# Optimization experiments

Hardware: AMD Instinct MI355X
Metric: run time of the kernel (lower is better)

Reference implementation:

```python
import jax, jax.numpy as jnp
import numpy as np

D = 64
NU = 30000
NI = 20000
LU = 50  # mailbox length at user nodes (item_max_length)
LI = 50  # mailbox length at item nodes (user_max_length)


def setup_inputs() -> dict:
    key = jax.random.key(0)
    ks = jax.random.split(key, 14)
    s = 0.05
    return {
        "user_feat": jax.random.normal(ks[0], (NU, D), jnp.float32),
        "item_feat": jax.random.normal(ks[1], (NI, D), jnp.float32),
        "W_u": jax.random.normal(ks[2], (D, D), jnp.float32) * s,
        "W_i": jax.random.normal(ks[3], (D, D), jnp.float32) * s,
        "Wg_u": jax.random.normal(ks[4], (2 * D, D), jnp.float32) * s,
        "Wg_i": jax.random.normal(ks[5], (2 * D, D), jnp.float32) * s,
        "i_te": jax.random.normal(ks[6], (LI, D), jnp.float32) * s,
        "i_te_k": jax.random.normal(ks[7], (LI, D), jnp.float32) * s,
        "u_te": jax.random.normal(ks[8], (LU, D), jnp.float32) * s,
        "u_te_k": jax.random.normal(ks[9], (LU, D), jnp.float32) * s,
        "item_nbr": jax.random.randint(ks[10], (NI, LI), 0, NU, jnp.int32),
        "item_time": jax.random.randint(ks[11], (NI, LI), 0, 1000000, jnp.int32),
        "user_nbr": jax.random.randint(ks[12], (NU, LU), 0, NI, jnp.int32),
        "user_time": jax.random.randint(ks[13], (NU, LU), 0, 1000000, jnp.int32),
    }


def _orgat_att(src_mb, dst_h, time, te, te_k):
    """One DGSR reduce: long-term time-encoded attention + short-term last-attention.
    src_mb: [N, L, d] gathered source features; dst_h: [N, d]; time: [N, L] int.
    Returns concat([h_long, h_short]) @ Wg applied by caller.
    """
    L = time.shape[1]
    d = src_mb.shape[-1]
    scale = jnp.sqrt(jnp.asarray(d, src_mb.dtype))
    # rank of each edge's time within the neighborhood; re_order: 0 = most recent
    rank = jnp.argsort(jnp.argsort(time, axis=1), axis=1)
    re_o = L - rank - 1                                       # [N, L]
    e = jnp.sum((te[re_o] + src_mb) * dst_h[:, None, :], axis=2) / scale
    alpha = jax.nn.softmax(e, axis=1)                         # [N, L]
    h_long = jnp.sum(alpha[..., None] * (src_mb + te_k[re_o]), axis=1)
    # short-term: attention keyed on the most-recent neighbor
    last = jnp.argmax(time, axis=1)
    last_em = jnp.take_along_axis(src_mb, last[:, None, None], axis=1)  # [N,1,d]
    e1 = jnp.sum(last_em * src_mb, axis=2) / scale
    a1 = jax.nn.softmax(e1, axis=1)
    h_short = jnp.sum(a1[..., None] * src_mb, axis=1)
    return jnp.concatenate([h_long, h_short], axis=-1)        # [N, 2d]


def reference(user_feat, item_feat, W_u, W_i, Wg_u, Wg_i, i_te, i_te_k,
              u_te, u_te_k, item_nbr, item_time, user_nbr, user_time):
    uh = user_feat @ W_u   # user_weight (feat_drop=0)
    ih = item_feat @ W_i   # item_weight
    # 'by' edges: users -> items (item reduce uses user mailboxes + i_time_encoding)
    u_mb = uh[item_nbr]                                        # [NI, LI, d]
    item_new = _orgat_att(u_mb, ih, item_time, i_te, i_te_k) @ Wg_i
    # 'pby' edges: items -> users (user reduce uses item mailboxes + u_time_encoding)
    i_mb = ih[user_nbr]                                        # [NU, LU, d]
    user_new = _orgat_att(i_mb, uh, user_time, u_te, u_te_k) @ Wg_u
    # residual update functions
    user_out = jax.nn.elu(user_new + user_feat)
    item_out = jax.nn.elu(item_new + item_feat)
    return user_out, item_out
```

## Files before the change

### kernel.cpp

```cpp
#include <hip/hip_runtime.h>
#include <stdint.h>

#define D   64
#define L   50
#define NUM_U 30000
#define NUM_I 20000
#define MROWS 50
#define PW3 (MROWS * 32 + 96 + 192)
#define GEMM_BLKS 782


typedef __attribute__((ext_vector_type(8))) short short8x;
typedef __attribute__((ext_vector_type(4))) float f32x4;

__device__ __forceinline__ float lof(unsigned int u) {
    union { unsigned int i; float f; } v; v.i = u << 16; return v.f;
}
__device__ __forceinline__ float hif(unsigned int u) {
    union { unsigned int i; float f; } v; v.i = u & 0xffff0000u; return v.f;
}
__device__ __forceinline__ unsigned int f2bfbits(float f) {
    union { float f; unsigned int i; } v; v.f = f;
    return (v.i + 0x7fffu + ((v.i >> 16) & 1u)) >> 16;
}
__device__ __forceinline__ unsigned int packbf(float a, float b) {
    return f2bfbits(a) | (f2bfbits(b) << 16);
}
__device__ __forceinline__ float rl(float v, int l) {
    return __int_as_float(__builtin_amdgcn_readlane(__float_as_int(v), l));
}
__device__ __forceinline__ int rli(int v, int l) {
    return __builtin_amdgcn_readlane(v, l);
}
__device__ __forceinline__ void gload_lds16(const void* g, void* l) {
    __builtin_amdgcn_global_load_lds(
        (const __attribute__((address_space(1))) unsigned int*)g,
        (__attribute__((address_space(3))) unsigned int*)l, 16, 0, 0);
}

__global__ __launch_bounds__(256) void prep(
    const float* __restrict__ user_feat, const float* __restrict__ item_feat,
    const float* __restrict__ W_u, const float* __restrict__ W_i,
    const float* __restrict__ Wg_i, const float* __restrict__ Wg_u,
    const float* __restrict__ te_i, const float* __restrict__ te_u,
    const float* __restrict__ tk_i, const float* __restrict__ tk_u,
    unsigned int* __restrict__ H,
    unsigned short* __restrict__ WgPi, unsigned short* __restrict__ WgPu,
    unsigned short* __restrict__ tePi, unsigned short* __restrict__ tePu,
    unsigned short* __restrict__ tkPi, unsigned short* __restrict__ tkPu)
{
    const int tid = threadIdx.x;
    if (blockIdx.x < GEMM_BLKS) {
        const int lane = tid & 63, wid = tid >> 6;
        const int tile = blockIdx.x * 4 + wid;
        if (tile >= 3125) return;
        const int r0 = tile * 16;
        const float* src; const float* W;
        if (r0 < NUM_U) { src = user_feat + (size_t)r0 * D;            W = W_u; }
        else            { src = item_feat + (size_t)(r0 - NUM_U) * D;  W = W_i; }
        const int q4 = lane >> 4, c16 = lane & 15;

        short8x bf[2];
#pragma unroll
        for (int kt = 0; kt < 2; kt++) {
            const float* fp = src + c16 * D + kt * 32 + q4 * 8;
            float4 x = *(const float4*)fp;
            float4 y = *(const float4*)(fp + 4);
            union { short8x v; unsigned int u[4]; } t2;
            t2.u[0] = packbf(x.x, x.y); t2.u[1] = packbf(x.z, x.w);
            t2.u[2] = packbf(y.x, y.y); t2.u[3] = packbf(y.z, y.w);
            bf[kt] = t2.v;
        }
        f32x4 zero4 = {0.f, 0.f, 0.f, 0.f};
        f32x4 acc[4];
#pragma unroll
        for (int mt = 0; mt < 4; mt++) acc[mt] = zero4;
#pragma unroll
        for (int kt = 0; kt < 2; kt++) {
#pragma unroll
            for (int mt = 0; mt < 4; mt++) {
                union { short8x v; unsigned short u[8]; } a;
#pragma unroll
                for (int j = 0; j < 8; j++)
                    a.u[j] = (unsigned short)f2bfbits(
                        W[(kt * 32 + q4 * 8 + j) * D + c16 + 16 * mt]);
                acc[mt] = __builtin_amdgcn_mfma_f32_16x16x32_bf16(a.v, bf[kt], acc[mt], 0, 0, 0);
            }
        }
        unsigned int* Hrow = H + (size_t)(r0 + c16) * 32;
#pragma unroll
        for (int mt = 0; mt < 4; mt++) {
            uint2 pk;
            pk.x = packbf(acc[mt][0], acc[mt][1]);
            pk.y = packbf(acc[mt][2], acc[mt][3]);
            *(uint2*)(Hrow + 8 * mt + 2 * q4) = pk;
        }
    } else {
        int gid = (blockIdx.x - GEMM_BLKS) * 256 + tid;
        for (int idx = gid; idx < 8192; idx += 4096) {
            int n = idx >> 7, k = idx & 127;
            WgPi[idx] = (unsigned short)f2bfbits(Wg_i[k * 64 + n]);
            WgPu[idx] = (unsigned short)f2bfbits(Wg_u[k * 64 + n]);
        }
        {
            int idx = gid;
            int r = idx >> 6, k = idx & 63;
            tePi[idx] = (r < L) ? (unsigned short)f2bfbits(te_i[r * 64 + k]) : 0;
            tePu[idx] = (r < L) ? (unsigned short)f2bfbits(te_u[r * 64 + k]) : 0;
            int d = idx >> 6, rr = idx & 63;
            tkPi[idx] = (rr < L) ? (unsigned short)f2bfbits(tk_i[rr * 64 + d]) : 0;
            tkPu[idx] = (rr < L) ? (unsigned short)f2bfbits(tk_u[rr * 64 + d]) : 0;
        }
    }
}

__global__ __launch_bounds__(256, 5) void attn_fused(
    const unsigned int* __restrict__ H,
    const float* __restrict__ user_feat, const float* __restrict__ item_feat,
    const unsigned short* __restrict__ WgPi, const unsigned short* __restrict__ WgPu,
    const unsigned short* __restrict__ tePi, const unsigned short* __restrict__ tePu,
    const unsigned short* __restrict__ tkPi, const unsigned short* __restrict__ tkPu,
    const int* __restrict__ item_nbr, const int* __restrict__ item_time,
    const int* __restrict__ user_nbr, const int* __restrict__ user_time,
    float* __restrict__ out)
{
    __shared__ unsigned int lds[4 * PW3];

    const int tid = threadIdx.x, lane = tid & 63, wid = tid >> 6;
    const bool iside = blockIdx.x < (NUM_I / 4);
    const int bb = iside ? blockIdx.x : blockIdx.x - NUM_I / 4;
    const int n = bb * 4 + wid;
    const int src_base = iside ? 0 : NUM_U;
    const int dst_base = iside ? NUM_U : 0;
    const float* dst_feat = iside ? item_feat : user_feat;
    const unsigned short* WgP  = iside ? WgPi : WgPu;
    const unsigned short* teP  = iside ? tePi : tePu;
    const unsigned short* tekP = iside ? tkPi : tkPu;
    const int* nbr   = iside ? item_nbr  : user_nbr;
    const int* timev = iside ? item_time : user_time;
    float* outp = out + (iside ? (size_t)NUM_U * D : 0);

    const int q4 = lane >> 4, c16 = lane & 15;

    const unsigned int*   Hsrc = H + (size_t)src_base * 32;
    const unsigned short* Hs16 = (const unsigned short*)H + (size_t)src_base * 64;
    const unsigned short* Hd16 = (const unsigned short*)H + (size_t)dst_base * 64;

    unsigned int*   wld  = lds + wid * PW3;
    unsigned int*   mbw  = wld;
    unsigned short* dla  = (unsigned short*)(wld + MROWS * 32);
    float*          escf = (float*)(wld + MROWS * 32 + 96);
    unsigned short* cat  = (unsigned short*)(wld + MROWS * 32 + 96);

    int t   = (lane < L) ? timev[(size_t)n * L + lane] : 0;
    int nbv = (lane < L) ? nbr[(size_t)n * L + lane]  : 0;

    {
        const int soff = (((lane & 7) ^ (lane >> 3)) << 4);
        const int rsel = (lane >> 3) << 2;
#pragma unroll
        for (int g = 0; g < 6; g++) {
            int nb = __builtin_amdgcn_ds_bpermute(rsel + (g << 5), nbv);
            const char* gp = (const char*)(Hsrc + (size_t)(unsigned)nb * 32)
                             + (soff ^ ((g & 3) << 5));
            gload_lds16(gp, (char*)mbw + (g << 10));
        }
        int row = 48 + (lane >> 5), d = lane & 31;
        int nb = __builtin_amdgcn_ds_bpermute(row << 2, nbv);
        unsigned int v = Hsrc[(size_t)(unsigned)nb * 32 + d];
        int swzr = (row & 7) ^ (((row >> 3) & 3) << 1);
        mbw[(row << 5) + ((((d >> 2) ^ swzr) << 2) | (d & 3))] = v;
    }

    short8x bKr[2][4];
#pragma unroll
    for (int kt = 0; kt < 2; kt++)
#pragma unroll
        for (int nt = 0; nt < 4; nt++)
            bKr[kt][nt] = *(const short8x*)(tekP + (c16 + 16 * nt) * 64
                                            + kt * 32 + q4 * 8);

    unsigned int key2 = (lane < L) ? ((((unsigned)t) << 6) | (unsigned)(63 - lane)) : 0u;
    unsigned int m2 = key2;
#pragma unroll
    for (int s = 32; s; s >>= 1) { unsigned int o2 = __shfl_xor(m2, s); m2 = (o2 > m2) ? o2 : m2; }
    const int last = 63 - (int)(m2 & 63u);
    int nbl = __shfl(nbv, last);

    short8x dhf[2], lmf[2];
#pragma unroll
    for (int kt = 0; kt < 2; kt++) {
        dhf[kt] = *(const short8x*)(Hd16 + (size_t)n * 64 + kt * 32 + q4 * 8);
        lmf[kt] = *(const short8x*)(Hs16 + (size_t)(unsigned)nbl * 64 + kt * 32 + q4 * 8);
    }

    unsigned int key = (lane < L) ? ((((unsigned)t) << 6) | (unsigned)lane) : 0u;
    int rank = 0;
#pragma unroll
    for (int j = 0; j < L; j++) {
        unsigned int kj = (unsigned int)rli((int)key, j);
        rank += (kj < key) ? 1 : 0;
    }
    int re_o = (lane < L) ? (L - 1 - rank) : lane;

    f32x4 zero4 = {0.f, 0.f, 0.f, 0.f};
    f32x4 acc_e[4], acc_t[4];
#pragma unroll
    for (int nt = 0; nt < 4; nt++) { acc_e[nt] = zero4; acc_t[nt] = zero4; }
    __builtin_amdgcn_s_setprio(1);
#pragma unroll
    for (int kt = 0; kt < 2; kt++) {
        short8x afr = (c16 & 1) ? lmf[kt] : dhf[kt];
        int cc = kt * 4 + q4;
#pragma unroll
        for (int nt = 0; nt < 4; nt++) {
            int row = c16 + 16 * nt;
            int rowc = (row < MROWS) ? row : 0;
            int swzr = (rowc & 7) ^ (((rowc >> 3) & 3) << 1);
            short8x bv = *(const short8x*)((const char*)mbw + rowc * 128
                                           + ((cc ^ swzr) << 4));
            acc_e[nt] = __builtin_amdgcn_mfma_f32_16x16x32_bf16(afr, bv, acc_e[nt], 0, 0, 0);
            short8x bt = *(const short8x*)(teP + row * 64 + kt * 32 + q4 * 8);
            acc_t[nt] = __builtin_amdgcn_mfma_f32_16x16x32_bf16(afr, bt, acc_t[nt], 0, 0, 0);
        }
    }
    __builtin_amdgcn_s_setprio(0);
    if (q4 == 0) {
#pragma unroll
        for (int nt = 0; nt < 4; nt++) {
            escf[c16 + 16 * nt]       = acc_e[nt][0];
            escf[64 + c16 + 16 * nt]  = acc_e[nt][1];
            escf[128 + c16 + 16 * nt] = acc_t[nt][0];
        }
    }
    float e  = escf[lane];
    float e1 = escf[64 + lane];
    float th = escf[128 + re_o];

    e = (e + th) * 0.125f;
    e1 *= 0.125f;
    if (lane >= L) { e = -3e38f; e1 = -3e38f; }

    float mx = e;
#pragma unroll
    for (int s = 32; s; s >>= 1) { float o2 = __shfl_xor(mx, s); mx = (o2 > mx) ? o2 : mx; }
    float ex = __expf(e - mx);
    float sm = ex;
#pragma unroll
    for (int s = 32; s; s >>= 1) sm += __shfl_xor(sm, s);
    float alpha = ex / sm;

    float mx1 = e1;
#pragma unroll
    for (int s = 32; s; s >>= 1) { float o2 = __shfl_xor(mx1, s); mx1 = (o2 > mx1) ? o2 : mx1; }
    float ex1 = __expf(e1 - mx1);
    float sm1 = ex1;
#pragma unroll
    for (int s = 32; s; s >>= 1) sm1 += __shfl_xor(sm1, s);
    float aw = ex1 / sm1;

    dla[lane]       = (unsigned short)f2bfbits(alpha);
    dla[64 + lane]  = (unsigned short)f2bfbits(aw);
    dla[128 + re_o] = (unsigned short)f2bfbits(alpha);

    f32x4 acc_s[4], acc_k[4];
#pragma unroll
    for (int nt = 0; nt < 4; nt++) { acc_s[nt] = zero4; acc_k[nt] = zero4; }
    __builtin_amdgcn_s_setprio(1);
#pragma unroll
    for (int kt = 0; kt < 2; kt++) {
        short8x aS = *(const short8x*)(dla + (c16 & 1) * 64 + kt * 32 + q4 * 8);
        short8x aB = *(const short8x*)(dla + 128 + kt * 32 + q4 * 8);
        int kr128[8];
#pragma unroll
        for (int i = 0; i < 8; i++) {
            int k = kt * 32 + q4 * 8 + i;
            if (kt) k = (k < MROWS) ? k : (k - 32);
            kr128[i] = k << 7;
        }
        const int qx = q4 << 1;
#pragma unroll
        for (int nt = 0; nt < 4; nt++) {
            int dc = c16 + 16 * nt;
            int tq = (dc >> 3) ^ qx;
            const char* cbase = (const char*)mbw + ((dc & 7) << 1);
            union { short8x v; unsigned short u[8]; } bu;
#pragma unroll
            for (int i = 0; i < 8; i++)
                bu.u[i] = *(const unsigned short*)(cbase + kr128[i] + ((tq ^ i) << 4));
            acc_s[nt] = __builtin_amdgcn_mfma_f32_16x16x32_bf16(aS, bu.v, acc_s[nt], 0, 0, 0);
            acc_k[nt] = __builtin_amdgcn_mfma_f32_16x16x32_bf16(aB, bKr[kt][nt], acc_k[nt], 0, 0, 0);
        }
    }
    __builtin_amdgcn_s_setprio(0);
    if (q4 == 0) {
#pragma unroll
        for (int nt = 0; nt < 4; nt++) {
            cat[c16 + 16 * nt]      = (unsigned short)f2bfbits(acc_s[nt][0] + acc_k[nt][0]);
            cat[64 + c16 + 16 * nt] = (unsigned short)f2bfbits(acc_s[nt][1]);
        }
    }
    __syncthreads();

    short8x bfr[4];
#pragma unroll
    for (int tK = 0; tK < 4; tK++)
        bfr[tK] = *(const short8x*)(WgP + (wid * 16 + c16) * 128 + tK * 32 + q4 * 8);

    const unsigned short* catw =
        (const unsigned short*)(lds + (lane & 3) * PW3 + MROWS * 32 + 96);
    f32x4 acc = zero4;
#pragma unroll
    for (int tK = 0; tK < 4; tK++) {
        short8x a = *(const short8x*)(catw + tK * 32 + q4 * 8);
        acc = __builtin_amdgcn_mfma_f32_16x16x32_bf16(a, bfr[tK], acc, 0, 0, 0);
    }
    float r01 = (q4 & 1) ? acc[1] : acc[0];
    float r23 = (q4 & 1) ? acc[3] : acc[2];
    float pv  = (q4 & 2) ? r23 : r01;

    int node = bb * 4 + q4;
    float fres = dst_feat[(size_t)node * D + wid * 16 + c16];
    float oo = pv + fres;
    oo = (oo > 0.f) ? oo : (__expf(oo) - 1.f);
    outp[(size_t)node * D + wid * 16 + c16] = oo;
}

__global__ __launch_bounds__(256) void attn_mono(
    const float* __restrict__ src_feat, const float* __restrict__ dst_feat,
    const float* __restrict__ W_src, const float* __restrict__ W_dst,
    const float* __restrict__ Wg, const float* __restrict__ te,
    const float* __restrict__ tek, const int* __restrict__ nbr,
    const int* __restrict__ timev, float* __restrict__ out)
{
    __shared__ unsigned int ws32[64 * 33];
    __shared__ unsigned int te32[L * 33];
    __shared__ unsigned int mbs[4][L * 33];
    const int tid = threadIdx.x, lane = tid & 63, wid = tid >> 6;
    const int n = blockIdx.x * 4 + wid;
    {
        const float2* Wf2 = (const float2*)W_src;
        const float2* Te2 = (const float2*)te;
        for (int idx = tid; idx < 2048; idx += 256) {
            float2 w = Wf2[idx];
            ws32[(idx >> 5) * 33 + (idx & 31)] = packbf(w.x, w.y);
            if (idx < 1600) {
                float2 t2 = Te2[idx];
                te32[(idx >> 5) * 33 + (idx & 31)] = packbf(t2.x, t2.y);
            }
        }
    }
    __syncthreads();
    int t  = (lane < L) ? timev[(size_t)n * L + lane] : 0;
    int nb = (lane < L) ? nbr[(size_t)n * L + lane]  : 0;
    unsigned int key  = (lane < L) ? ((((unsigned)t) << 6) | (unsigned)lane) : 0u;
    unsigned int key2 = (lane < L) ? ((((unsigned)t) << 6) | (unsigned)(63 - lane)) : 0u;
    int rank = 0;
#pragma unroll
    for (int j = 0; j < L; j++) {
        unsigned int kj = (unsigned int)rli((int)key, j);
        rank += (kj < key) ? 1 : 0;
    }
    int re_o = (lane < L) ? (L - 1 - rank) : 0;
    unsigned int m2 = key2;
#pragma unroll
    for (int s = 32; s; s >>= 1) { unsigned int o2 = __shfl_xor(m2, s); m2 = (o2 > m2) ? o2 : m2; }
    const int last = 63 - (int)(m2 & 63u);
    const int rr = (lane < L) ? lane : (L - 1);
    float f = dst_feat[(size_t)n * D + lane];
    float dh;
    {
        float b0 = 0.f, b1 = 0.f, b2 = 0.f, b3 = 0.f;
#pragma unroll
        for (int k = 0; k < 64; k += 4) {
            b0 += rl(f, k + 0) * W_dst[(k + 0) * 64 + lane];
            b1 += rl(f, k + 1) * W_dst[(k + 1) * 64 + lane];
            b2 += rl(f, k + 2) * W_dst[(k + 2) * 64 + lane];
            b3 += rl(f, k + 3) * W_dst[(k + 3) * 64 + lane];
        }
        dh = (b0 + b1) + (b2 + b3);
    }
    float v1;
    {
        float b0 = 0.f, b1 = 0.f, b2 = 0.f, b3 = 0.f;
#pragma unroll
        for (int j = 0; j < 32; j += 2) {
            unsigned int u0 = ws32[lane * 33 + j];
            unsigned int u1 = ws32[lane * 33 + j + 1];
            b0 += lof(u0) * rl(dh, 2 * j + 0);
            b1 += hif(u0) * rl(dh, 2 * j + 1);
            b2 += lof(u1) * rl(dh, 2 * j + 2);
            b3 += hif(u1) * rl(dh, 2 * j + 3);
        }
        v1 = (b0 + b1) + (b2 + b3);
    }
    unsigned int* mbw = mbs[wid];
    {
        const float2* src2 = (const float2*)src_feat;
        int half = lane >> 5, col = lane & 31;
#pragma unroll
        for (int l = 0; l < L; l += 2) {
            int ra = rli(nb, l), rb = rli(nb, l + 1);
            int r = half ? rb : ra;
            float2 v = src2[(size_t)r * 32 + col];
            mbw[(l + half) * 33 + col] = packbf(v.x, v.y);
        }
    }
    __syncthreads();
    unsigned int ul = mbw[last * 33 + (lane >> 1)];
    float rlast = (lane & 1) ? hif(ul) : lof(ul);
    float g;
    {
        float b0 = 0.f, b1 = 0.f, b2 = 0.f, b3 = 0.f;
#pragma unroll
        for (int k = 0; k < 64; k += 4) {
            b0 += rl(rlast, k + 0) * W_src[(k + 0) * 64 + lane];
            b1 += rl(rlast, k + 1) * W_src[(k + 1) * 64 + lane];
            b2 += rl(rlast, k + 2) * W_src[(k + 2) * 64 + lane];
            b3 += rl(rlast, k + 3) * W_src[(k + 3) * 64 + lane];
        }
        g = (b0 + b1) + (b2 + b3);
    }
    float v2;
    {
        float b0 = 0.f, b1 = 0.f, b2 = 0.f, b3 = 0.f;
#pragma unroll
        for (int j = 0; j < 32; j += 2) {
            unsigned int u0 = ws32[lane * 33 + j];
            unsigned int u1 = ws32[lane * 33 + j + 1];
            b0 += lof(u0) * rl(g, 2 * j + 0);
            b1 += hif(u0) * rl(g, 2 * j + 1);
            b2 += lof(u1) * rl(g, 2 * j + 2);
            b3 += hif(u1) * rl(g, 2 * j + 3);
        }
        v2 = (b0 + b1) + (b2 + b3);
    }
    float teh;
    {
        float b0 = 0.f, b1 = 0.f, b2 = 0.f, b3 = 0.f;
#pragma unroll
        for (int j = 0; j < 32; j += 2) {
            unsigned int u0 = te32[rr * 33 + j];
            unsigned int u1 = te32[rr * 33 + j + 1];
            b0 += lof(u0) * rl(dh, 2 * j + 0);
            b1 += hif(u0) * rl(dh, 2 * j + 1);
            b2 += lof(u1) * rl(dh, 2 * j + 2);
            b3 += hif(u1) * rl(dh, 2 * j + 3);
        }
        teh = (b0 + b1) + (b2 + b3);
    }
    float e, e1;
    {
        float ea = 0.f, eb = 0.f, qa = 0.f, qb = 0.f;
#pragma unroll
        for (int j = 0; j < 32; j += 2) {
            unsigned int u0 = mbw[rr * 33 + j];
            unsigned int u1 = mbw[rr * 33 + j + 1];
            float m0 = lof(u0), m1 = hif(u0), m2f = lof(u1), m3 = hif(u1);
            ea += m0 * rl(v1, 2 * j + 0) + m1 * rl(v1, 2 * j + 1);
            eb += m2f * rl(v1, 2 * j + 2) + m3 * rl(v1, 2 * j + 3);
            qa += m0 * rl(v2, 2 * j + 0) + m1 * rl(v2, 2 * j + 1);
            qb += m2f * rl(v2, 2 * j + 2) + m3 * rl(v2, 2 * j + 3);
        }
        e = ea + eb; e1 = qa + qb;
    }
    e = (e + __shfl(teh, re_o)) * 0.125f;
    e1 *= 0.125f;
    if (lane >= L) { e = -3e38f; e1 = -3e38f; }
    float mx = e;
#pragma unroll
    for (int s = 32; s; s >>= 1) { float o2 = __shfl_xor(mx, s); mx = (o2 > mx) ? o2 : mx; }
    float ex = __expf(e - mx);
    float sm = ex;
#pragma unroll
    for (int s = 32; s; s >>= 1) sm += __shfl_xor(sm, s);
    float alpha = ex / sm;
    float mx1 = e1;
#pragma unroll
    for (int s = 32; s; s >>= 1) { float o2 = __shfl_xor(mx1, s); mx1 = (o2 > mx1) ? o2 : mx1; }
    float ex1 = __expf(e1 - mx1);
    float sm1 = ex1;
#pragma unroll
    for (int s = 32; s; s >>= 1) sm1 += __shfl_xor(sm1, s);
    float aw = ex1 / sm1;
    float sl, ss, tacc;
    {
        float sA = 0.f, sB = 0.f, hA = 0.f, hB = 0.f, tA = 0.f, tB = 0.f;
        int hcol = lane >> 1, odd = lane & 1;
#pragma unroll
        for (int l = 0; l < L; l += 2) {
            float saA = rl(alpha, l),     s1A = rl(aw, l);
            float saB = rl(alpha, l + 1), s1B = rl(aw, l + 1);
            int   roA = rli(re_o, l),     roB = rli(re_o, l + 1);
            unsigned int uA = mbw[(l + 0) * 33 + hcol];
            unsigned int uB = mbw[(l + 1) * 33 + hcol];
            float mA = odd ? hif(uA) : lof(uA);
            float mB = odd ? hif(uB) : lof(uB);
            sA += saA * mA; hA += s1A * mA; tA += saA * tek[roA * 64 + lane];
            sB += saB * mB; hB += s1B * mB; tB += saB * tek[roB * 64 + lane];
        }
        sl = sA + sB; ss = hA + hB; tacc = tA + tB;
    }
    float hl, hs;
    {
        float lA = 0.f, lB = 0.f, sA = 0.f, sB = 0.f;
#pragma unroll
        for (int k = 0; k < 64; k += 2) {
            float w0 = W_src[(k + 0) * 64 + lane];
            float w1 = W_src[(k + 1) * 64 + lane];
            lA += rl(sl, k + 0) * w0; sA += rl(ss, k + 0) * w0;
            lB += rl(sl, k + 1) * w1; sB += rl(ss, k + 1) * w1;
        }
        hl = tacc + lA + lB; hs = sA + sB;
    }
    float o;
    {
        float o0 = 0.f, o1 = 0.f, o2 = 0.f, o3 = 0.f;
#pragma unroll
        for (int k = 0; k < 64; k += 2) {
            o0 += rl(hl, k + 0) * Wg[(k + 0) * 64 + lane];
            o1 += rl(hl, k + 1) * Wg[(k + 1) * 64 + lane];
            o2 += rl(hs, k + 0) * Wg[(k + 64) * 64 + lane];
            o3 += rl(hs, k + 1) * Wg[(k + 65) * 64 + lane];
        }
        o = f + (o0 + o1) + (o2 + o3);
    }
    o = (o > 0.f) ? o : (__expf(o) - 1.f);
    out[(size_t)n * D + lane] = o;
}

extern "C" void kernel_launch(void* const* d_in, const int* in_sizes, int n_in,
                              void* d_out, int out_size, void* d_ws, size_t ws_size,
                              hipStream_t stream) {
    const float* user_feat = (const float*)d_in[0];
    const float* item_feat = (const float*)d_in[1];
    const float* W_u  = (const float*)d_in[2];
    const float* W_i  = (const float*)d_in[3];
    const float* Wg_u = (const float*)d_in[4];
    const float* Wg_i = (const float*)d_in[5];
    const float* i_te   = (const float*)d_in[6];
    const float* i_te_k = (const float*)d_in[7];
    const float* u_te   = (const float*)d_in[8];
    const float* u_te_k = (const float*)d_in[9];
    const int* item_nbr  = (const int*)d_in[10];
    const int* item_time = (const int*)d_in[11];
    const int* user_nbr  = (const int*)d_in[12];
    const int* user_time = (const int*)d_in[13];
    (void)in_sizes; (void)n_in; (void)out_size;

    float* outp = (float*)d_out;
    const size_t H_BYTES = (size_t)(NUM_U + NUM_I) * 32 * 4;
    const size_t NEED = H_BYTES + 2 * 16384 + 4 * 8192;

    if (ws_size >= NEED) {
        unsigned int* Hp = (unsigned int*)d_ws;
        unsigned char* aux = (unsigned char*)d_ws + H_BYTES;
        unsigned short* WgPi = (unsigned short*)(aux);
        unsigned short* WgPu = (unsigned short*)(aux + 16384);
        unsigned short* tePi = (unsigned short*)(aux + 32768);
        unsigned short* tePu = (unsigned short*)(aux + 40960);
        unsigned short* tkPi = (unsigned short*)(aux + 49152);
        unsigned short* tkPu = (unsigned short*)(aux + 57344);

        prep<<<GEMM_BLKS + 16, 256, 0, stream>>>(user_feat, item_feat, W_u, W_i,
                                       Wg_i, Wg_u, i_te, u_te, i_te_k, u_te_k,
                                       Hp, WgPi, WgPu, tePi, tePu, tkPi, tkPu);
        attn_fused<<<(NUM_I + NUM_U) / 4, 256, 0, stream>>>(
            Hp, user_feat, item_feat, WgPi, WgPu, tePi, tePu, tkPi, tkPu,
            item_nbr, item_time, user_nbr, user_time, outp);
    } else {
        attn_mono<<<NUM_I / 4, 256, 0, stream>>>(
            user_feat, item_feat, W_u, W_i, Wg_i, i_te, i_te_k,
            item_nbr, item_time, outp + (size_t)NUM_U * D);
        attn_mono<<<NUM_U / 4, 256, 0, stream>>>(
            item_feat, user_feat, W_i, W_u, Wg_u, u_te, u_te_k,
            user_nbr, user_time, outp);
    }
}
```

Before: 252.6 us.

## Shrink LDS and registers in attn_fused to fit six blocks per CU

Per-wave LDS shrinks by dropping the float score scratch area: attention scores are now redistributed across lanes with shuffles and a 4-way select instead of an LDS round trip. The dst and last-neighbour feature fragments are staged through LDS rather than held in registers. The time-key B fragments are loaded from global memory inside the MFMA loop instead of being preloaded into registers, and launch bounds rise from 5 to 6 blocks per CU. The aim is higher occupancy to hide gather latency, at the cost of extra shuffles and global loads on the critical path.

```diff
diff --git a/kernel.cpp b/kernel.cpp
--- a/kernel.cpp
+++ b/kernel.cpp
@@ -6,7 +6,8 @@
 #define NUM_U 30000
 #define NUM_I 20000
 #define MROWS 50
-#define PW3 (MROWS * 32 + 96 + 192)
+#define REG_OFF 1600
+#define PW3 1696
 #define GEMM_BLKS 782
 
 
@@ -36,6 +37,11 @@
     __builtin_amdgcn_global_load_lds(
         (const __attribute__((address_space(1))) unsigned int*)g,
         (__attribute__((address_space(3))) unsigned int*)l, 16, 0, 0);
+}
+__device__ __forceinline__ float sel4(float v0, float v1, float v2, float v3, int idx) {
+    float a = (idx & 1) ? v1 : v0;
+    float b = (idx & 1) ? v3 : v2;
+    return (idx & 2) ? b : a;
 }
 
 __global__ __launch_bounds__(256) void prep(
@@ -114,7 +120,7 @@
     }
 }
 
-__global__ __launch_bounds__(256, 5) void attn_fused(
+__global__ __launch_bounds__(256, 6) void attn_fused(
     const unsigned int* __restrict__ H,
     const float* __restrict__ user_feat, const float* __restrict__ item_feat,
     const unsigned short* __restrict__ WgPi, const unsigned short* __restrict__ WgPu,
@@ -146,11 +152,10 @@
     const unsigned short* Hs16 = (const unsigned short*)H + (size_t)src_base * 64;
     const unsigned short* Hd16 = (const unsigned short*)H + (size_t)dst_base * 64;
 
-    unsigned int*   wld  = lds + wid * PW3;
-    unsigned int*   mbw  = wld;
-    unsigned short* dla  = (unsigned short*)(wld + MROWS * 32);
-    float*          escf = (float*)(wld + MROWS * 32 + 96);
-    unsigned short* cat  = (unsigned short*)(wld + MROWS * 32 + 96);
+    unsigned int*   wld = lds + wid * PW3;
+    unsigned int*   mbw = wld;
+    unsigned short* dla = (unsigned short*)(wld + REG_OFF);
+    unsigned short* cat = (unsigned short*)(wld + REG_OFF);
 
     int t   = (lane < L) ? timev[(size_t)n * L + lane] : 0;
     int nbv = (lane < L) ? nbr[(size_t)n * L + lane]  : 0;
@@ -172,27 +177,14 @@
         mbw[(row << 5) + ((((d >> 2) ^ swzr) << 2) | (d & 3))] = v;
     }
 
-    short8x bKr[2][4];
-#pragma unroll
-    for (int kt = 0; kt < 2; kt++)
-#pragma unroll
-        for (int nt = 0; nt < 4; nt++)
-            bKr[kt][nt] = *(const short8x*)(tekP + (c16 + 16 * nt) * 64
-                                            + kt * 32 + q4 * 8);
-
     unsigned int key2 = (lane < L) ? ((((unsigned)t) << 6) | (unsigned)(63 - lane)) : 0u;
     unsigned int m2 = key2;
 #pragma unroll
     for (int s = 32; s; s >>= 1) { unsigned int o2 = __shfl_xor(m2, s); m2 = (o2 > m2) ? o2 : m2; }
     const int last = 63 - (int)(m2 & 63u);
     int nbl = __shfl(nbv, last);
-
-    short8x dhf[2], lmf[2];
-#pragma unroll
-    for (int kt = 0; kt < 2; kt++) {
-        dhf[kt] = *(const short8x*)(Hd16 + (size_t)n * 64 + kt * 32 + q4 * 8);
-        lmf[kt] = *(const short8x*)(Hs16 + (size_t)(unsigned)nbl * 64 + kt * 32 + q4 * 8);
-    }
+    unsigned short dh_u = Hd16[(size_t)n * 64 + lane];
+    unsigned short lm_u = Hs16[(size_t)(unsigned)nbl * 64 + lane];
 
     unsigned int key = (lane < L) ? ((((unsigned)t) << 6) | (unsigned)lane) : 0u;
     int rank = 0;
@@ -203,6 +195,9 @@
     }
     int re_o = (lane < L) ? (L - 1 - rank) : lane;
 
+    dla[lane]      = dh_u;
+    dla[64 + lane] = lm_u;
+
     f32x4 zero4 = {0.f, 0.f, 0.f, 0.f};
     f32x4 acc_e[4], acc_t[4];
 #pragma unroll
@@ -210,7 +205,7 @@
     __builtin_amdgcn_s_setprio(1);
 #pragma unroll
     for (int kt = 0; kt < 2; kt++) {
-        short8x afr = (c16 & 1) ? lmf[kt] : dhf[kt];
+        short8x afr = *(const short8x*)(dla + (c16 & 1) * 64 + kt * 32 + q4 * 8);
         int cc = kt * 4 + q4;
 #pragma unroll
         for (int nt = 0; nt < 4; nt++) {
@@ -225,17 +220,17 @@
         }
     }
     __builtin_amdgcn_s_setprio(0);
-    if (q4 == 0) {
-#pragma unroll
-        for (int nt = 0; nt < 4; nt++) {
-            escf[c16 + 16 * nt]       = acc_e[nt][0];
-            escf[64 + c16 + 16 * nt]  = acc_e[nt][1];
-            escf[128 + c16 + 16 * nt] = acc_t[nt][0];
-        }
-    }
-    float e  = escf[lane];
-    float e1 = escf[64 + lane];
-    float th = escf[128 + re_o];
+
+    float eN0  = __shfl(acc_e[0][0], c16), eN1  = __shfl(acc_e[1][0], c16);
+    float eN2  = __shfl(acc_e[2][0], c16), eN3  = __shfl(acc_e[3][0], c16);
+    float f1N0 = __shfl(acc_e[0][1], c16), f1N1 = __shfl(acc_e[1][1], c16);
+    float f1N2 = __shfl(acc_e[2][1], c16), f1N3 = __shfl(acc_e[3][1], c16);
+    int rsrc = re_o & 15;
+    float tN0 = __shfl(acc_t[0][0], rsrc), tN1 = __shfl(acc_t[1][0], rsrc);
+    float tN2 = __shfl(acc_t[2][0], rsrc), tN3 = __shfl(acc_t[3][0], rsrc);
+    float e  = sel4(eN0, eN1, eN2, eN3, q4);
+    float e1 = sel4(f1N0, f1N1, f1N2, f1N3, q4);
+    float th = sel4(tN0, tN1, tN2, tN3, (re_o >> 4) & 3);
 
     e = (e + th) * 0.125f;
     e1 *= 0.125f;
@@ -289,7 +284,8 @@
             for (int i = 0; i < 8; i++)
                 bu.u[i] = *(const unsigned short*)(cbase + kr128[i] + ((tq ^ i) << 4));
             acc_s[nt] = __builtin_amdgcn_mfma_f32_16x16x32_bf16(aS, bu.v, acc_s[nt], 0, 0, 0);
-            acc_k[nt] = __builtin_amdgcn_mfma_f32_16x16x32_bf16(aB, bKr[kt][nt], acc_k[nt], 0, 0, 0);
+            short8x bK = *(const short8x*)(tekP + dc * 64 + kt * 32 + q4 * 8);
+            acc_k[nt] = __builtin_amdgcn_mfma_f32_16x16x32_bf16(aB, bK, acc_k[nt], 0, 0, 0);
         }
     }
     __builtin_amdgcn_s_setprio(0);
@@ -308,7 +304,7 @@
         bfr[tK] = *(const short8x*)(WgP + (wid * 16 + c16) * 128 + tK * 32 + q4 * 8);
 
     const unsigned short* catw =
-        (const unsigned short*)(lds + (lane & 3) * PW3 + MROWS * 32 + 96);
+        (const unsigned short*)(lds + (lane & 3) * PW3 + REG_OFF);
     f32x4 acc = zero4;
 #pragma unroll
     for (int tK = 0; tK < 4; tK++) {
```

After: 231.7 us. -8.3%, faster.

## Precompute per-node time-encoding dot products in prep kernel

Applied to the files above, without the earlier changes.

The prep GEMM kernel now also computes te·dst_h for every node and time slot (a 64-wide table per node) with MFMA and writes it to workspace. The attention kernel reads one value per lane instead of running the te MFMA chain, and it loads dst/last embeddings through LDS rather than holding them as register fragments. It also stops keeping the te_k B-fragments in registers and reloads them from global memory inside the loop. This cuts MFMA work and register pressure in the hot kernel. In exchange it adds a 12.8 MB fp32 write and read through HBM, and the new path only runs when the workspace is large enough.

```diff
diff --git a/kernel.cpp b/kernel.cpp
--- a/kernel.cpp
+++ b/kernel.cpp
@@ -6,7 +6,8 @@
 #define NUM_U 30000
 #define NUM_I 20000
 #define MROWS 50
-#define PW3 (MROWS * 32 + 96 + 192)
+#define REG_OFF 1600
+#define PW3 1888
 #define GEMM_BLKS 782
 
 
@@ -44,7 +45,7 @@
     const float* __restrict__ Wg_i, const float* __restrict__ Wg_u,
     const float* __restrict__ te_i, const float* __restrict__ te_u,
     const float* __restrict__ tk_i, const float* __restrict__ tk_u,
-    unsigned int* __restrict__ H,
+    unsigned int* __restrict__ H, float* __restrict__ tehT,
     unsigned short* __restrict__ WgPi, unsigned short* __restrict__ WgPu,
     unsigned short* __restrict__ tePi, unsigned short* __restrict__ tePu,
     unsigned short* __restrict__ tkPi, unsigned short* __restrict__ tkPu)
@@ -55,9 +56,9 @@
         const int tile = blockIdx.x * 4 + wid;
         if (tile >= 3125) return;
         const int r0 = tile * 16;
-        const float* src; const float* W;
-        if (r0 < NUM_U) { src = user_feat + (size_t)r0 * D;            W = W_u; }
-        else            { src = item_feat + (size_t)(r0 - NUM_U) * D;  W = W_i; }
+        const float* src; const float* W; const float* teD;
+        if (r0 < NUM_U) { src = user_feat + (size_t)r0 * D;           W = W_u; teD = te_u; }
+        else            { src = item_feat + (size_t)(r0 - NUM_U) * D; W = W_i; teD = te_i; }
         const int q4 = lane >> 4, c16 = lane & 15;
 
         short8x bf[2];
@@ -95,6 +96,34 @@
             pk.y = packbf(acc[mt][2], acc[mt][3]);
             *(uint2*)(Hrow + 8 * mt + 2 * q4) = pk;
         }
+
+        if (tehT) {
+            asm volatile("s_waitcnt vmcnt(0)" ::: "memory");
+            const char* Hb = (const char*)(H + (size_t)r0 * 32);
+            short8x hb0 = *(const short8x*)(Hb + c16 * 128 + 0 * 64 + q4 * 16);
+            short8x hb1 = *(const short8x*)(Hb + c16 * 128 + 1 * 64 + q4 * 16);
+#pragma unroll
+            for (int mt = 0; mt < 4; mt++) {
+                f32x4 at = zero4;
+                const int rowm = c16 + 16 * mt;
+                union { short8x v; unsigned short u[8]; } a;
+#pragma unroll
+                for (int j = 0; j < 8; j++) {
+                    int k = q4 * 8 + j;
+                    a.u[j] = (rowm < L) ? (unsigned short)f2bfbits(teD[rowm * 64 + k])
+                                        : (unsigned short)0;
+                }
+                at = __builtin_amdgcn_mfma_f32_16x16x32_bf16(a.v, hb0, at, 0, 0, 0);
+#pragma unroll
+                for (int j = 0; j < 8; j++) {
+                    int k = 32 + q4 * 8 + j;
+                    a.u[j] = (rowm < L) ? (unsigned short)f2bfbits(teD[rowm * 64 + k])
+                                        : (unsigned short)0;
+                }
+                at = __builtin_amdgcn_mfma_f32_16x16x32_bf16(a.v, hb1, at, 0, 0, 0);
+                *(f32x4*)(tehT + (size_t)(r0 + c16) * 64 + 16 * mt + 4 * q4) = at;
+            }
+        }
     } else {
         int gid = (blockIdx.x - GEMM_BLKS) * 256 + tid;
         for (int idx = gid; idx < 8192; idx += 4096) {
@@ -122,7 +151,7 @@
     const unsigned short* __restrict__ tkPi, const unsigned short* __restrict__ tkPu,
     const int* __restrict__ item_nbr, const int* __restrict__ item_time,
     const int* __restrict__ user_nbr, const int* __restrict__ user_time,
-    float* __restrict__ out)
+    const float* __restrict__ tehT, float* __restrict__ out)
 {
     __shared__ unsigned int lds[4 * PW3];
 
@@ -148,9 +177,9 @@
 
     unsigned int*   wld  = lds + wid * PW3;
     unsigned int*   mbw  = wld;
-    unsigned short* dla  = (unsigned short*)(wld + MROWS * 32);
-    float*          escf = (float*)(wld + MROWS * 32 + 96);
-    unsigned short* cat  = (unsigned short*)(wld + MROWS * 32 + 96);
+    unsigned short* dla  = (unsigned short*)(wld + REG_OFF);
+    float*          escf = (float*)(wld + REG_OFF + 96);
+    unsigned short* cat  = (unsigned short*)(wld + REG_OFF + 96);
 
     int t   = (lane < L) ? timev[(size_t)n * L + lane] : 0;
     int nbv = (lane < L) ? nbr[(size_t)n * L + lane]  : 0;
@@ -172,27 +201,14 @@
         mbw[(row << 5) + ((((d >> 2) ^ swzr) << 2) | (d & 3))] = v;
     }
 
-    short8x bKr[2][4];
-#pragma unroll
-    for (int kt = 0; kt < 2; kt++)
-#pragma unroll
-        for (int nt = 0; nt < 4; nt++)
-            bKr[kt][nt] = *(const short8x*)(tekP + (c16 + 16 * nt) * 64
-                                            + kt * 32 + q4 * 8);
-
     unsigned int key2 = (lane < L) ? ((((unsigned)t) << 6) | (unsigned)(63 - lane)) : 0u;
     unsigned int m2 = key2;
 #pragma unroll
     for (int s = 32; s; s >>= 1) { unsigned int o2 = __shfl_xor(m2, s); m2 = (o2 > m2) ? o2 : m2; }
     const int last = 63 - (int)(m2 & 63u);
     int nbl = __shfl(nbv, last);
-
-    short8x dhf[2], lmf[2];
-#pragma unroll
-    for (int kt = 0; kt < 2; kt++) {
-        dhf[kt] = *(const short8x*)(Hd16 + (size_t)n * 64 + kt * 32 + q4 * 8);
-        lmf[kt] = *(const short8x*)(Hs16 + (size_t)(unsigned)nbl * 64 + kt * 32 + q4 * 8);
-    }
+    unsigned short dh_u = Hd16[(size_t)n * 64 + lane];
+    unsigned short lm_u = Hs16[(size_t)(unsigned)nbl * 64 + lane];
 
     unsigned int key = (lane < L) ? ((((unsigned)t) << 6) | (unsigned)lane) : 0u;
     int rank = 0;
@@ -203,39 +219,70 @@
     }
     int re_o = (lane < L) ? (L - 1 - rank) : lane;
 
+    float th = 0.f;
+    if (tehT) th = tehT[(size_t)(dst_base + n) * 64 + re_o];
+
+    dla[lane]      = dh_u;
+    dla[64 + lane] = lm_u;
+
     f32x4 zero4 = {0.f, 0.f, 0.f, 0.f};
-    f32x4 acc_e[4], acc_t[4];
-#pragma unroll
-    for (int nt = 0; nt < 4; nt++) { acc_e[nt] = zero4; acc_t[nt] = zero4; }
-    __builtin_amdgcn_s_setprio(1);
-#pragma unroll
-    for (int kt = 0; kt < 2; kt++) {
-        short8x afr = (c16 & 1) ? lmf[kt] : dhf[kt];
-        int cc = kt * 4 + q4;
+    f32x4 acc_e[4];
+#pragma unroll
+    for (int nt = 0; nt < 4; nt++) acc_e[nt] = zero4;
+    if (tehT) {
+        __builtin_amdgcn_s_setprio(1);
+#pragma unroll
+        for (int kt = 0; kt < 2; kt++) {
+            short8x afr = *(const short8x*)(dla + (c16 & 1) * 64 + kt * 32 + q4 * 8);
+            int cc = kt * 4 + q4;
+#pragma unroll
+            for (int nt = 0; nt < 4; nt++) {
+                int row = c16 + 16 * nt;
+                int rowc = (row < MROWS) ? row : 0;
+                int swzr = (rowc & 7) ^ (((rowc >> 3) & 3) << 1);
+                short8x bv = *(const short8x*)((const char*)mbw + rowc * 128
+                                               + ((cc ^ swzr) << 4));
+                acc_e[nt] = __builtin_amdgcn_mfma_f32_16x16x32_bf16(afr, bv, acc_e[nt], 0, 0, 0);
+            }
+        }
+        __builtin_amdgcn_s_setprio(0);
+    } else {
+        f32x4 acc_t[4];
+#pragma unroll
+        for (int nt = 0; nt < 4; nt++) acc_t[nt] = zero4;
+        __builtin_amdgcn_s_setprio(1);
+#pragma unroll
+        for (int kt = 0; kt < 2; kt++) {
+            short8x afr = *(const short8x*)(dla + (c16 & 1) * 64 + kt * 32 + q4 * 8);
+            int cc = kt * 4 + q4;
+#pragma unroll
+            for (int nt = 0; nt < 4; nt++) {
+                int row = c16 + 16 * nt;
+                int rowc = (row < MROWS) ? row : 0;
+                int swzr = (rowc & 7) ^ (((rowc >> 3) & 3) << 1);
+                short8x bv = *(const short8x*)((const char*)mbw + rowc * 128
+                                               + ((cc ^ swzr) << 4));
+                acc_e[nt] = __builtin_amdgcn_mfma_f32_16x16x32_bf16(afr, bv, acc_e[nt], 0, 0, 0);
+                short8x bt = *(const short8x*)(teP + row * 64 + kt * 32 + q4 * 8);
+                acc_t[nt] = __builtin_amdgcn_mfma_f32_16x16x32_bf16(afr, bt, acc_t[nt], 0, 0, 0);
+            }
+        }
+        __builtin_amdgcn_s_setprio(0);
+        if (q4 == 0) {
+#pragma unroll
+            for (int nt = 0; nt < 4; nt++) escf[128 + c16 + 16 * nt] = acc_t[nt][0];
+        }
+    }
+    if (q4 == 0) {
 #pragma unroll
         for (int nt = 0; nt < 4; nt++) {
-            int row = c16 + 16 * nt;
-            int rowc = (row < MROWS) ? row : 0;
-            int swzr = (rowc & 7) ^ (((rowc >> 3) & 3) << 1);
-            short8x bv = *(const short8x*)((const char*)mbw + rowc * 128
-                                           + ((cc ^ swzr) << 4));
-            acc_e[nt] = __builtin_amdgcn_mfma_f32_16x16x32_bf16(afr, bv, acc_e[nt], 0, 0, 0);
-            short8x bt = *(const short8x*)(teP + row * 64 + kt * 32 + q4 * 8);
-            acc_t[nt] = __builtin_amdgcn_mfma_f32_16x16x32_bf16(afr, bt, acc_t[nt], 0, 0, 0);
-        }
-    }
-    __builtin_amdgcn_s_setprio(0);
-    if (q4 == 0) {
-#pragma unroll
-        for (int nt = 0; nt < 4; nt++) {
-            escf[c16 + 16 * nt]       = acc_e[nt][0];
-            escf[64 + c16 + 16 * nt]  = acc_e[nt][1];
-            escf[128 + c16 + 16 * nt] = acc_t[nt][0];
+            escf[c16 + 16 * nt]      = acc_e[nt][0];
+            escf[64 + c16 + 16 * nt] = acc_e[nt][1];
         }
     }
     float e  = escf[lane];
     float e1 = escf[64 + lane];
-    float th = escf[128 + re_o];
+    if (!tehT) th = escf[128 + re_o];
 
     e = (e + th) * 0.125f;
     e1 *= 0.125f;
@@ -289,7 +336,8 @@
             for (int i = 0; i < 8; i++)
                 bu.u[i] = *(const unsigned short*)(cbase + kr128[i] + ((tq ^ i) << 4));
             acc_s[nt] = __builtin_amdgcn_mfma_f32_16x16x32_bf16(aS, bu.v, acc_s[nt], 0, 0, 0);
-            acc_k[nt] = __builtin_amdgcn_mfma_f32_16x16x32_bf16(aB, bKr[kt][nt], acc_k[nt], 0, 0, 0);
+            short8x bK = *(const short8x*)(tekP + dc * 64 + kt * 32 + q4 * 8);
+            acc_k[nt] = __builtin_amdgcn_mfma_f32_16x16x32_bf16(aB, bK, acc_k[nt], 0, 0, 0);
         }
     }
     __builtin_amdgcn_s_setprio(0);
@@ -308,7 +356,7 @@
         bfr[tK] = *(const short8x*)(WgP + (wid * 16 + c16) * 128 + tK * 32 + q4 * 8);
 
     const unsigned short* catw =
-        (const unsigned short*)(lds + (lane & 3) * PW3 + MROWS * 32 + 96);
+        (const unsigned short*)(lds + (lane & 3) * PW3 + REG_OFF + 96);
     f32x4 acc = zero4;
 #pragma unroll
     for (int tK = 0; tK < 4; tK++) {
@@ -549,8 +597,11 @@
     (void)in_sizes; (void)n_in; (void)out_size;
 
     float* outp = (float*)d_out;
-    const size_t H_BYTES = (size_t)(NUM_U + NUM_I) * 32 * 4;
-    const size_t NEED = H_BYTES + 2 * 16384 + 4 * 8192;
+    const size_t H_BYTES   = (size_t)(NUM_U + NUM_I) * 32 * 4;
+    const size_t AUX_BYTES = 2 * 16384 + 4 * 8192;
+    const size_t TEH_BYTES = (size_t)(NUM_U + NUM_I) * 64 * 4;
+    const size_t NEED  = H_BYTES + AUX_BYTES;
+    const size_t NEED2 = NEED + TEH_BYTES;
 
     if (ws_size >= NEED) {
         unsigned int* Hp = (unsigned int*)d_ws;
@@ -561,13 +612,16 @@
         unsigned short* tePu = (unsigned short*)(aux + 40960);
         unsigned short* tkPi = (unsigned short*)(aux + 49152);
         unsigned short* tkPu = (unsigned short*)(aux + 57344);
+        float* tehp = (ws_size >= NEED2)
+                      ? (float*)((unsigned char*)d_ws + H_BYTES + AUX_BYTES)
+                      : (float*)nullptr;
 
         prep<<<GEMM_BLKS + 16, 256, 0, stream>>>(user_feat, item_feat, W_u, W_i,
                                        Wg_i, Wg_u, i_te, u_te, i_te_k, u_te_k,
-                                       Hp, WgPi, WgPu, tePi, tePu, tkPi, tkPu);
+                                       Hp, tehp, WgPi, WgPu, tePi, tePu, tkPi, tkPu);
         attn_fused<<<(NUM_I + NUM_U) / 4, 256, 0, stream>>>(
             Hp, user_feat, item_feat, WgPi, WgPu, tePi, tePu, tkPi, tkPu,
-            item_nbr, item_time, user_nbr, user_time, outp);
+            item_nbr, item_time, user_nbr, user_time, tehp, outp);
     } else {
         attn_mono<<<NUM_I / 4, 256, 0, stream>>>(
             user_feat, item_feat, W_u, W_i, Wg_i, i_te, i_te_k,
```

Result: faster. 203.7 us (-19.4%).
